# Kernel tuning notes

Measured on AMD Instinct MI355X. Metric: run time of the kernel, lower is better.

Reference implementation:

```python
import jax, jax.numpy as jnp
import numpy as np
import math

N, KZ, IFZ, AHZ, AFZ = 20000, 16, 256, 8, 32
EPS = 1e-5


def layernorm(x, g, b):
    m = jnp.mean(x, axis=-1, keepdims=True)
    v = jnp.mean((x - m) ** 2, axis=-1, keepdims=True)
    return (x - m) * jax.lax.rsqrt(v + EPS) * g + b


def rotate_half(x):
    x1, x2 = jnp.split(x, 2, axis=-1)
    return jnp.concatenate([-x2, x1], axis=-1)


def setup_inputs() -> dict:
    key = jax.random.key(0)
    ks = jax.random.split(key, 16)
    s = 1.0 / math.sqrt(IFZ)
    hf = AHZ * AFZ
    return {
        "x_1": jax.random.normal(ks[0], (N, IFZ), jnp.float32),
        "x_2": jax.random.normal(ks[1], (N, KZ, IFZ), jnp.float32),
        "pos_emb": jax.random.normal(ks[2], (N, AFZ), jnp.float32),
        "edge_index": jax.random.randint(ks[3], (N, KZ), 0, N),
        "Wq": jax.random.normal(ks[4], (IFZ, hf), jnp.float32) * s,
        "Wk": jax.random.normal(ks[5], (IFZ, hf), jnp.float32) * s,
        "Wv": jax.random.normal(ks[6], (IFZ, hf), jnp.float32) * s,
        "Wb": jax.random.normal(ks[7], (IFZ, AHZ), jnp.float32) * s,
        "bln_g": jnp.ones((IFZ,), jnp.float32),
        "bln_b": jnp.zeros((IFZ,), jnp.float32),
        "Wg": jax.random.normal(ks[8], (IFZ, hf), jnp.float32) * s,
        "bg": jnp.zeros((hf,), jnp.float32),
        "Wback": jax.random.normal(ks[9], (hf, IFZ), jnp.float32) / math.sqrt(hf),
        "bback": jnp.zeros((IFZ,), jnp.float32),
        "ln1_g": jnp.ones((IFZ,), jnp.float32),
        "ln1_b": jnp.zeros((IFZ,), jnp.float32),
    }


def reference(x_1, x_2, pos_emb, edge_index, Wq, Wk, Wv, Wb, bln_g, bln_b,
              Wg, bg, Wback, bback, ln1_g, ln1_b):
    n = x_1.shape[0]
    y_1 = x_1[edge_index]                                  # [N,kz,ifz] irregular gather
    q = (x_1 @ Wq).reshape(n, AHZ, AFZ)                    # [N,h,f]
    k = (y_1 @ Wk).reshape(n, KZ, AHZ, AFZ)                # [N,kz,h,f]
    # RoPE: rotate q by each node's own angles, k by gathered neighbor angles
    cos_q = jnp.cos(pos_emb)[:, None, :]                   # [N,1,f]
    sin_q = jnp.sin(pos_emb)[:, None, :]
    q = q * cos_q + rotate_half(q) * sin_q
    pe_n = pos_emb[edge_index]                             # [N,kz,f]
    cos_k = jnp.cos(pe_n)[:, :, None, :]                   # [N,kz,1,f]
    sin_k = jnp.sin(pe_n)[:, :, None, :]
    k = k * cos_k + rotate_half(k) * sin_k
    v = (y_1 @ Wv).reshape(n, KZ, AHZ, AFZ)
    bias_2 = layernorm(x_2, bln_g, bln_b) @ Wb             # [N,kz,h]
    gate = jax.nn.sigmoid(x_1 @ Wg + bg).reshape(n, AHZ, AFZ)
    scores = jnp.einsum('nhf,nkhf->nkh', q, k) / math.sqrt(AFZ) + bias_2
    w = jax.nn.softmax(scores, axis=1)                     # over kz neighbors
    out = gate * jnp.einsum('nkh,nkhf->nhf', w, v)         # [N,h,f]
    out = out.reshape(n, AHZ * AFZ) @ Wback + bback + math.sqrt(2.0) * x_1
    return layernorm(out, ln1_g, ln1_b)
```

## Files before the change

### kernel.cpp

```cpp
#include <hip/hip_runtime.h>
#include <math.h>

#define IFZ 256
#define KZ  16
#define AHZ 8
#define AFZ 32
#define HF  256

typedef _Float16 half8 __attribute__((ext_vector_type(8)));
typedef _Float16 half4 __attribute__((ext_vector_type(4)));
typedef float    f32x4 __attribute__((ext_vector_type(4)));

__global__ void conv_f16(const float* __restrict__ in, _Float16* __restrict__ out, int n4)
{
    int i = blockIdx.x * 256 + threadIdx.x;
    if (i >= n4) return;
    float4 v = reinterpret_cast<const float4*>(in)[i];
    half4 h;
    h[0] = (_Float16)v.x; h[1] = (_Float16)v.y;
    h[2] = (_Float16)v.z; h[3] = (_Float16)v.w;
    reinterpret_cast<half4*>(out)[i] = h;
}

__global__ void prep_all(const float* __restrict__ w0, const float* __restrict__ w1,
                         const float* __restrict__ w2, const float* __restrict__ w3,
                         const float* __restrict__ w4, _Float16* __restrict__ out,
                         const float* __restrict__ g, const float* __restrict__ b,
                         const float* __restrict__ Wb,
                         _Float16* __restrict__ c1T, float* __restrict__ c23)
{
    const int m = blockIdx.y;
    if (m < 5) {
        int k = blockIdx.x;
        int c = threadIdx.x;
        const float* w = (m == 0) ? w0 : (m == 1) ? w1 : (m == 2) ? w2 : (m == 3) ? w3 : w4;
        out[(size_t)m * 65536 + (size_t)c * 256 + k] = (_Float16)w[(size_t)k * 256 + c];
        return;
    }
    if (blockIdx.x != 0) return;

    __shared__ float red[4][16];
    const int f = threadIdx.x;
    const int w = f >> 6, l = f & 63;
    const float gv = g[f], bv = b[f];
    float ph2[8], ph3[8];
    #pragma unroll
    for (int h = 0; h < 8; ++h) {
        float wv = Wb[(size_t)f * 8 + h];
        c1T[h * 256 + f] = (_Float16)(gv * wv);
        ph2[h] = gv * wv;
        ph3[h] = bv * wv;
    }
    c1T[8 * 256 + f] = (_Float16)1.0f;
    #pragma unroll
    for (int cc = 9; cc < 16; ++cc) c1T[cc * 256 + f] = (_Float16)0.0f;

    #pragma unroll
    for (int h = 0; h < 8; ++h) {
        #pragma unroll
        for (int o = 32; o > 0; o >>= 1) {
            ph2[h] += __shfl_xor(ph2[h], o);
            ph3[h] += __shfl_xor(ph3[h], o);
        }
        if (l == h) { red[w][h] = ph2[h]; red[w][8 + h] = ph3[h]; }
    }
    __syncthreads();
    if (f < 16) c23[f] = red[0][f] + red[1][f] + red[2][f] + red[3][f];
}

__launch_bounds__(256)
__global__ void gemm_qkvg(const _Float16* __restrict__ A, const _Float16* __restrict__ WT,
                          const float* __restrict__ pe, const float* __restrict__ bg,
                          _Float16* __restrict__ QH, _Float16* __restrict__ KH,
                          _Float16* __restrict__ VH, _Float16* __restrict__ GH, int N)
{
    __shared__ _Float16 as[64][40];
    __shared__ _Float16 bs[4][64][40];

    const int tid = threadIdx.x;
    const int l   = tid & 63;
    const int w   = tid >> 6;
    const int n0  = blockIdx.x * 64;
    const int c0  = blockIdx.y * 64;

    f32x4 acc[4][4];
    #pragma unroll
    for (int m = 0; m < 4; ++m)
        #pragma unroll
        for (int b = 0; b < 4; ++b)
            { acc[m][b][0]=0.f; acc[m][b][1]=0.f; acc[m][b][2]=0.f; acc[m][b][3]=0.f; }

    const int srow = tid >> 2;
    const int sch  = (tid & 3) * 8;
    const size_t aoff = (size_t)(n0 + srow) * IFZ + sch;
    const size_t boff = (size_t)(c0 + srow) * IFZ + sch;

    half8 av{}, bv0, bv1, bv2, bv3;
    if (n0 + srow < N) av = *reinterpret_cast<const half8*>(A + aoff);
    bv0 = *reinterpret_cast<const half8*>(WT + 0 * 65536 + boff);
    bv1 = *reinterpret_cast<const half8*>(WT + 1 * 65536 + boff);
    bv2 = *reinterpret_cast<const half8*>(WT + 2 * 65536 + boff);
    bv3 = *reinterpret_cast<const half8*>(WT + 3 * 65536 + boff);

    for (int kt = 0; kt < 8; ++kt) {
        __syncthreads();
        *reinterpret_cast<half8*>(&as[srow][sch])    = av;
        *reinterpret_cast<half8*>(&bs[0][srow][sch]) = bv0;
        *reinterpret_cast<half8*>(&bs[1][srow][sch]) = bv1;
        *reinterpret_cast<half8*>(&bs[2][srow][sch]) = bv2;
        *reinterpret_cast<half8*>(&bs[3][srow][sch]) = bv3;
        __syncthreads();

        half8 nav{}, nbv0{}, nbv1{}, nbv2{}, nbv3{};
        if (kt < 7) {
            const int k0 = (kt + 1) * 32;
            if (n0 + srow < N) nav = *reinterpret_cast<const half8*>(A + aoff + k0);
            nbv0 = *reinterpret_cast<const half8*>(WT + 0 * 65536 + boff + k0);
            nbv1 = *reinterpret_cast<const half8*>(WT + 1 * 65536 + boff + k0);
            nbv2 = *reinterpret_cast<const half8*>(WT + 2 * 65536 + boff + k0);
            nbv3 = *reinterpret_cast<const half8*>(WT + 3 * 65536 + boff + k0);
        }

        half8 af = *reinterpret_cast<const half8*>(&as[16 * w + (l & 15)][8 * (l >> 4)]);
        #pragma unroll
        for (int m = 0; m < 4; ++m) {
            #pragma unroll
            for (int b = 0; b < 4; ++b) {
                half8 bf = *reinterpret_cast<const half8*>(&bs[m][16 * b + (l & 15)][8 * (l >> 4)]);
                acc[m][b] = __builtin_amdgcn_mfma_f32_16x16x32_f16(af, bf, acc[m][b], 0, 0, 0);
            }
        }
        av = nav; bv0 = nbv0; bv1 = nbv1; bv2 = nbv2; bv3 = nbv3;
    }

    #pragma unroll
    for (int r = 0; r < 4; ++r) {
        const int grow = n0 + 16 * w + ((l >> 4) << 2) + r;
        if (grow >= N) continue;
        float a0 = pe[(size_t)grow * AFZ + (l & 15)];
        float a1 = pe[(size_t)grow * AFZ + 16 + (l & 15)];
        float s0, c0f, s1, c1f;
        __sincosf(a0, &s0, &c0f);
        __sincosf(a1, &s1, &c1f);
        #pragma unroll
        for (int m = 0; m < 2; ++m) {
            _Float16* o = m ? KH : QH;
            #pragma unroll
            for (int pb = 0; pb < 4; pb += 2) {
                float v0 = acc[m][pb][r], v1 = acc[m][pb + 1][r];
                o[(size_t)grow * HF + c0 + 16 * pb       + (l & 15)] = (_Float16)(v0 * c0f - v1 * s0);
                o[(size_t)grow * HF + c0 + 16 * (pb + 1) + (l & 15)] = (_Float16)(v1 * c1f + v0 * s1);
            }
        }
        #pragma unroll
        for (int b = 0; b < 4; ++b)
            VH[(size_t)grow * HF + c0 + 16 * b + (l & 15)] = (_Float16)acc[2][b][r];
        #pragma unroll
        for (int b = 0; b < 4; ++b) {
            const int c = c0 + 16 * b + (l & 15);
            float v = acc[3][b][r] + bg[c];
            GH[(size_t)grow * HF + c] = (_Float16)(1.f / (1.f + __expf(-v)));
        }
    }
}

__launch_bounds__(256)
__global__ void attn_fused(const _Float16* __restrict__ Qh, const _Float16* __restrict__ Kh,
                           const _Float16* __restrict__ Vh, const _Float16* __restrict__ Gh,
                           const int* __restrict__ eidx, const float* __restrict__ x2,
                           const _Float16* __restrict__ c1T, const float* __restrict__ c23,
                           _Float16* __restrict__ AOh, int N)
{
    const int tid = threadIdx.x;
    const int l   = tid & 63;
    const int w   = tid >> 6;
    const int n   = blockIdx.x * 4 + w;
    if (n >= N) return;
    const int h = l >> 3;
    const int c = l & 15;
    const int p = l >> 4;

    const int ei_reg = eidx[(size_t)n * KZ + c];

    const float* xr = x2 + ((size_t)n * KZ + c) * IFZ + p * 8;
    f32x4 xv[16];
    #pragma unroll
    for (int kt = 0; kt < 8; ++kt) {
        xv[2 * kt]     = __builtin_nontemporal_load(reinterpret_cast<const f32x4*>(xr + kt * 32));
        xv[2 * kt + 1] = __builtin_nontemporal_load(reinterpret_cast<const f32x4*>(xr + kt * 32 + 4));
    }
    half8 bf[8];
    #pragma unroll
    for (int kt = 0; kt < 8; ++kt)
        bf[kt] = *reinterpret_cast<const half8*>(c1T + (size_t)c * 256 + kt * 32 + p * 8);

    f32x4 acc1 = {0.f, 0.f, 0.f, 0.f};
    f32x4 acc2 = {0.f, 0.f, 0.f, 0.f};
    #pragma unroll
    for (int kt = 0; kt < 8; ++kt) {
        f32x4 xa = xv[2 * kt], xb = xv[2 * kt + 1];
        half8 ax, ax2;
        ax[0] = (_Float16)xa[0]; ax[1] = (_Float16)xa[1];
        ax[2] = (_Float16)xa[2]; ax[3] = (_Float16)xa[3];
        ax[4] = (_Float16)xb[0]; ax[5] = (_Float16)xb[1];
        ax[6] = (_Float16)xb[2]; ax[7] = (_Float16)xb[3];
        ax2[0] = (_Float16)(xa[0] * xa[0]); ax2[1] = (_Float16)(xa[1] * xa[1]);
        ax2[2] = (_Float16)(xa[2] * xa[2]); ax2[3] = (_Float16)(xa[3] * xa[3]);
        ax2[4] = (_Float16)(xb[0] * xb[0]); ax2[5] = (_Float16)(xb[1] * xb[1]);
        ax2[6] = (_Float16)(xb[2] * xb[2]); ax2[7] = (_Float16)(xb[3] * xb[3]);
        acc1 = __builtin_amdgcn_mfma_f32_16x16x32_f16(ax,  bf[kt], acc1, 0, 0, 0);
        acc2 = __builtin_amdgcn_mfma_f32_16x16x32_f16(ax2, bf[kt], acc2, 0, 0, 0);
    }

    const float c2v = (c < 8) ? c23[c]     : 0.f;
    const float c3v = (c < 8) ? c23[8 + c] : 0.f;
    const int srcl = (l & 48) | 8;
    float bval[4];
    #pragma unroll
    for (int j = 0; j < 4; ++j) {
        float s1 = __shfl(acc1[j], srcl);
        float s2 = __shfl(acc2[j], srcl);
        float m    = s1 * (1.f / 256.f);
        float var  = s2 * (1.f / 256.f) - m * m;
        float rstd = rsqrtf(var + 1e-5f);
        bval[j] = rstd * (acc1[j] - m * c2v) + c3v;
    }

    half4 qh4 = *reinterpret_cast<const half4*>(Qh + (size_t)n * HF + 4 * l);
    const float q0 = (float)qh4[0], q1 = (float)qh4[1],
                q2 = (float)qh4[2], q3 = (float)qh4[3];

    float sc[16];
    #pragma unroll
    for (int e = 0; e < 16; ++e) {
        const int row = __shfl(ei_reg, e);
        half4 kh4 = *reinterpret_cast<const half4*>(Kh + (size_t)row * HF + 4 * l);
        float s = q0 * (float)kh4[0] + q1 * (float)kh4[1]
                + q2 * (float)kh4[2] + q3 * (float)kh4[3];
        s += __shfl_xor(s, 1); s += __shfl_xor(s, 2); s += __shfl_xor(s, 4);
        sc[e] = s * 0.17677669529663687f
              + __shfl(bval[e & 3], ((e >> 2) << 4) | h);
    }

    float m = sc[0];
    #pragma unroll
    for (int e = 1; e < 16; ++e) m = fmaxf(m, sc[e]);
    float sum = 0.f;
    #pragma unroll
    for (int e = 0; e < 16; ++e) { sc[e] = __expf(sc[e] - m); sum += sc[e]; }
    const float inv = 1.f / sum;

    float o0 = 0.f, o1 = 0.f, o2 = 0.f, o3 = 0.f;
    #pragma unroll
    for (int e = 0; e < 16; ++e) {
        const int row = __shfl(ei_reg, e);
        half4 vh4 = *reinterpret_cast<const half4*>(Vh + (size_t)row * HF + 4 * l);
        const float we = sc[e] * inv;
        o0 = fmaf(we, (float)vh4[0], o0);
        o1 = fmaf(we, (float)vh4[1], o1);
        o2 = fmaf(we, (float)vh4[2], o2);
        o3 = fmaf(we, (float)vh4[3], o3);
    }

    half4 gh4 = *reinterpret_cast<const half4*>(Gh + (size_t)n * HF + 4 * l);
    half4 oh;
    oh[0] = (_Float16)(o0 * (float)gh4[0]);
    oh[1] = (_Float16)(o1 * (float)gh4[1]);
    oh[2] = (_Float16)(o2 * (float)gh4[2]);
    oh[3] = (_Float16)(o3 * (float)gh4[3]);
    *reinterpret_cast<half4*>(AOh + (size_t)n * HF + 4 * l) = oh;
}

__launch_bounds__(256)
__global__ void gemm_back(const _Float16* __restrict__ A, const _Float16* __restrict__ BT,
                          const float* __restrict__ bias, float* __restrict__ Y, int N)
{
    __shared__ _Float16 as[64][40];
    __shared__ _Float16 bs[64][40];

    const int tid = threadIdx.x;
    const int l   = tid & 63;
    const int w   = tid >> 6;
    const int n0  = blockIdx.x * 64;
    const int c0  = blockIdx.y * 64;

    f32x4 acc[4];
    #pragma unroll
    for (int b = 0; b < 4; ++b) { acc[b][0]=0.f; acc[b][1]=0.f; acc[b][2]=0.f; acc[b][3]=0.f; }

    const int srow = tid >> 2;
    const int sch  = (tid & 3) * 8;
    const size_t aoff = (size_t)(n0 + srow) * IFZ + sch;
    const size_t boff = (size_t)(c0 + srow) * IFZ + sch;

    half8 av{}, bv;
    if (n0 + srow < N) av = *reinterpret_cast<const half8*>(A + aoff);
    bv = *reinterpret_cast<const half8*>(BT + boff);

    for (int kt = 0; kt < 8; ++kt) {
        __syncthreads();
        *reinterpret_cast<half8*>(&as[srow][sch]) = av;
        *reinterpret_cast<half8*>(&bs[srow][sch]) = bv;
        __syncthreads();

        half8 nav{}, nbv{};
        if (kt < 7) {
            const int k0 = (kt + 1) * 32;
            if (n0 + srow < N) nav = *reinterpret_cast<const half8*>(A + aoff + k0);
            nbv = *reinterpret_cast<const half8*>(BT + boff + k0);
        }

        half8 af = *reinterpret_cast<const half8*>(&as[16 * w + (l & 15)][8 * (l >> 4)]);
        #pragma unroll
        for (int b = 0; b < 4; ++b) {
            half8 bf = *reinterpret_cast<const half8*>(&bs[16 * b + (l & 15)][8 * (l >> 4)]);
            acc[b] = __builtin_amdgcn_mfma_f32_16x16x32_f16(af, bf, acc[b], 0, 0, 0);
        }
        av = nav; bv = nbv;
    }

    #pragma unroll
    for (int r = 0; r < 4; ++r) {
        const int grow = n0 + 16 * w + ((l >> 4) << 2) + r;
        if (grow >= N) continue;
        #pragma unroll
        for (int b = 0; b < 4; ++b) {
            const int c = c0 + 16 * b + (l & 15);
            Y[(size_t)grow * HF + c] = acc[b][r] + bias[c];
        }
    }
}

__launch_bounds__(256)
__global__ void final_ln(const float* __restrict__ RAWb,
                         const float* __restrict__ x1b,
                         const float* __restrict__ g1,
                         const float* __restrict__ b1,
                         float* __restrict__ outb,
                         int N)
{
    int n    = blockIdx.x * 4 + (threadIdx.x >> 6);
    int lane = threadIdx.x & 63;
    if (n >= N) return;
    const size_t off = (size_t)n * IFZ + lane * 4;
    float4 ur = *reinterpret_cast<const float4*>(RAWb + off);
    float4 ux = *reinterpret_cast<const float4*>(x1b + off);
    float x[4];
    x[0] = ur.x + 1.4142135623730951f * ux.x;
    x[1] = ur.y + 1.4142135623730951f * ux.y;
    x[2] = ur.z + 1.4142135623730951f * ux.z;
    x[3] = ur.w + 1.4142135623730951f * ux.w;
    float s = x[0] + x[1] + x[2] + x[3];
    float q = x[0]*x[0] + x[1]*x[1] + x[2]*x[2] + x[3]*x[3];
    #pragma unroll
    for (int o = 32; o > 0; o >>= 1) { s += __shfl_xor(s, o); q += __shfl_xor(q, o); }
    float m    = s * (1.f / 256.f);
    float var  = q * (1.f / 256.f) - m * m;
    float rstd = rsqrtf(var + 1e-5f);
    float4 uo;
    {
        int f = lane * 4;
        uo.x = (x[0] - m) * rstd * g1[f + 0] + b1[f + 0];
        uo.y = (x[1] - m) * rstd * g1[f + 1] + b1[f + 1];
        uo.z = (x[2] - m) * rstd * g1[f + 2] + b1[f + 2];
        uo.w = (x[3] - m) * rstd * g1[f + 3] + b1[f + 3];
    }
    *reinterpret_cast<float4*>(outb + off) = uo;
}

extern "C" void kernel_launch(void* const* d_in, const int* in_sizes, int n_in,
                              void* d_out, int out_size, void* d_ws, size_t ws_size,
                              hipStream_t stream)
{
    const float* x1   = (const float*)d_in[0];
    const float* x2   = (const float*)d_in[1];
    const float* pe   = (const float*)d_in[2];
    const int*   ei   = (const int*)d_in[3];
    const float* wq   = (const float*)d_in[4];
    const float* wk   = (const float*)d_in[5];
    const float* wv   = (const float*)d_in[6];
    const float* wb   = (const float*)d_in[7];
    const float* blng = (const float*)d_in[8];
    const float* blnb = (const float*)d_in[9];
    const float* wg   = (const float*)d_in[10];
    const float* bg   = (const float*)d_in[11];
    const float* wbk  = (const float*)d_in[12];
    const float* bbk  = (const float*)d_in[13];
    const float* g1   = (const float*)d_in[14];
    const float* b1   = (const float*)d_in[15];

    const int N = in_sizes[0] / IFZ;

    const size_t S2 = (((size_t)N * HF * 2) + 4095) & ~(size_t)4095;
    char* base = (char*)d_ws;
    _Float16* X1H = (_Float16*)(base);
    _Float16* QH  = (_Float16*)(base + 1 * S2);
    _Float16* KH  = (_Float16*)(base + 2 * S2);
    _Float16* VH  = (_Float16*)(base + 3 * S2);
    _Float16* GH  = (_Float16*)(base + 4 * S2);
    _Float16* WT  = (_Float16*)(base + 5 * S2);
    _Float16* C1T = (_Float16*)(base + 5 * S2 + (1u << 20));
    float*    C23 = (float*)   (base + 5 * S2 + (1u << 20) + 8192);
    _Float16* AOH = QH;
    float*    RAW = (float*)(base + 2 * S2);

    conv_f16<<<dim3((N * IFZ / 4 + 255) / 256), 256, 0, stream>>>(x1, X1H, N * IFZ / 4);
    prep_all<<<dim3(256, 6), 256, 0, stream>>>(wq, wk, wv, wg, wbk, WT,
                                               blng, blnb, wb, C1T, C23);

    const int nt = (N + 63) / 64;
    gemm_qkvg<<<dim3(nt, 4), 256, 0, stream>>>(X1H, WT, pe, bg, QH, KH, VH, GH, N);

    attn_fused<<<dim3((N + 3) / 4), 256, 0, stream>>>(QH, KH, VH, GH, ei, x2,
                                                      C1T, C23, AOH, N);

    gemm_back<<<dim3(nt, 4), 256, 0, stream>>>(AOH, WT + 4 * 65536, bbk, RAW, N);

    final_ln<<<dim3((N + 3) / 4), 256, 0, stream>>>(RAW, x1, g1, b1, (float*)d_out, N);
}
```

Baseline: 168.3 us.

## Fuse f32-to-f16 conversion into QKVG GEMM and fuse output LayerNorm into back GEMM

Drops the separate conv_f16 kernel, so gemm_qkvg now loads x_1 in fp32 and converts it to f16 while staging tiles. gemm_back now gives each block the full 256 output columns, letting it add bias and the scaled residual and apply the final LayerNorm in registers with lane shuffles. This removes the fp32 RAW intermediate round trip and two kernel launches. In exchange, each back-GEMM block holds 16 accumulators and a larger shared tile, so register pressure rises and there are a quarter as many blocks (about 313). The epilogue also does strided per-element stores and x1 loads.

```diff
diff --git a/kernel.cpp b/kernel.cpp
--- a/kernel.cpp
+++ b/kernel.cpp
@@ -10,17 +10,6 @@
 typedef _Float16 half8 __attribute__((ext_vector_type(8)));
 typedef _Float16 half4 __attribute__((ext_vector_type(4)));
 typedef float    f32x4 __attribute__((ext_vector_type(4)));
-
-__global__ void conv_f16(const float* __restrict__ in, _Float16* __restrict__ out, int n4)
-{
-    int i = blockIdx.x * 256 + threadIdx.x;
-    if (i >= n4) return;
-    float4 v = reinterpret_cast<const float4*>(in)[i];
-    half4 h;
-    h[0] = (_Float16)v.x; h[1] = (_Float16)v.y;
-    h[2] = (_Float16)v.z; h[3] = (_Float16)v.w;
-    reinterpret_cast<half4*>(out)[i] = h;
-}
 
 __global__ void prep_all(const float* __restrict__ w0, const float* __restrict__ w1,
                          const float* __restrict__ w2, const float* __restrict__ w3,
@@ -69,7 +58,7 @@
 }
 
 __launch_bounds__(256)
-__global__ void gemm_qkvg(const _Float16* __restrict__ A, const _Float16* __restrict__ WT,
+__global__ void gemm_qkvg(const float* __restrict__ A, const _Float16* __restrict__ WT,
                           const float* __restrict__ pe, const float* __restrict__ bg,
                           _Float16* __restrict__ QH, _Float16* __restrict__ KH,
                           _Float16* __restrict__ VH, _Float16* __restrict__ GH, int N)
@@ -94,9 +83,15 @@
     const int sch  = (tid & 3) * 8;
     const size_t aoff = (size_t)(n0 + srow) * IFZ + sch;
     const size_t boff = (size_t)(c0 + srow) * IFZ + sch;
+    const bool arow_ok = (n0 + srow < N);
 
     half8 av{}, bv0, bv1, bv2, bv3;
-    if (n0 + srow < N) av = *reinterpret_cast<const half8*>(A + aoff);
+    if (arow_ok) {
+        f32x4 a0 = *reinterpret_cast<const f32x4*>(A + aoff);
+        f32x4 a1 = *reinterpret_cast<const f32x4*>(A + aoff + 4);
+        av[0]=(_Float16)a0[0]; av[1]=(_Float16)a0[1]; av[2]=(_Float16)a0[2]; av[3]=(_Float16)a0[3];
+        av[4]=(_Float16)a1[0]; av[5]=(_Float16)a1[1]; av[6]=(_Float16)a1[2]; av[7]=(_Float16)a1[3];
+    }
     bv0 = *reinterpret_cast<const half8*>(WT + 0 * 65536 + boff);
     bv1 = *reinterpret_cast<const half8*>(WT + 1 * 65536 + boff);
     bv2 = *reinterpret_cast<const half8*>(WT + 2 * 65536 + boff);
@@ -114,7 +109,12 @@
         half8 nav{}, nbv0{}, nbv1{}, nbv2{}, nbv3{};
         if (kt < 7) {
             const int k0 = (kt + 1) * 32;
-            if (n0 + srow < N) nav = *reinterpret_cast<const half8*>(A + aoff + k0);
+            if (arow_ok) {
+                f32x4 a0 = *reinterpret_cast<const f32x4*>(A + aoff + k0);
+                f32x4 a1 = *reinterpret_cast<const f32x4*>(A + aoff + k0 + 4);
+                nav[0]=(_Float16)a0[0]; nav[1]=(_Float16)a0[1]; nav[2]=(_Float16)a0[2]; nav[3]=(_Float16)a0[3];
+                nav[4]=(_Float16)a1[0]; nav[5]=(_Float16)a1[1]; nav[6]=(_Float16)a1[2]; nav[7]=(_Float16)a1[3];
+            }
             nbv0 = *reinterpret_cast<const half8*>(WT + 0 * 65536 + boff + k0);
             nbv1 = *reinterpret_cast<const half8*>(WT + 1 * 65536 + boff + k0);
             nbv2 = *reinterpret_cast<const half8*>(WT + 2 * 65536 + boff + k0);
@@ -272,100 +272,102 @@
 }
 
 __launch_bounds__(256)
-__global__ void gemm_back(const _Float16* __restrict__ A, const _Float16* __restrict__ BT,
-                          const float* __restrict__ bias, float* __restrict__ Y, int N)
+__global__ void gemm_back_ln(const _Float16* __restrict__ A, const _Float16* __restrict__ BT,
+                             const float* __restrict__ bbk, const float* __restrict__ x1,
+                             const float* __restrict__ g1, const float* __restrict__ b1,
+                             float* __restrict__ out, int N)
 {
     __shared__ _Float16 as[64][40];
-    __shared__ _Float16 bs[64][40];
+    __shared__ _Float16 bs[256][40];
 
     const int tid = threadIdx.x;
     const int l   = tid & 63;
     const int w   = tid >> 6;
     const int n0  = blockIdx.x * 64;
-    const int c0  = blockIdx.y * 64;
-
-    f32x4 acc[4];
-    #pragma unroll
-    for (int b = 0; b < 4; ++b) { acc[b][0]=0.f; acc[b][1]=0.f; acc[b][2]=0.f; acc[b][3]=0.f; }
-
-    const int srow = tid >> 2;
-    const int sch  = (tid & 3) * 8;
-    const size_t aoff = (size_t)(n0 + srow) * IFZ + sch;
-    const size_t boff = (size_t)(c0 + srow) * IFZ + sch;
-
-    half8 av{}, bv;
-    if (n0 + srow < N) av = *reinterpret_cast<const half8*>(A + aoff);
-    bv = *reinterpret_cast<const half8*>(BT + boff);
+
+    f32x4 acc[16];
+    #pragma unroll
+    for (int bb = 0; bb < 16; ++bb)
+        { acc[bb][0]=0.f; acc[bb][1]=0.f; acc[bb][2]=0.f; acc[bb][3]=0.f; }
+
+    const int srowA = tid >> 2;
+    const int schA  = (tid & 3) * 8;
+    const size_t aoff = (size_t)(n0 + srowA) * IFZ + schA;
+    const size_t boff = (size_t)tid * IFZ;
+    const bool arow_ok = (n0 + srowA < N);
+
+    half8 av{}, bv[4];
+    if (arow_ok) av = *reinterpret_cast<const half8*>(A + aoff);
+    #pragma unroll
+    for (int i = 0; i < 4; ++i)
+        bv[i] = *reinterpret_cast<const half8*>(BT + boff + i * 8);
 
     for (int kt = 0; kt < 8; ++kt) {
         __syncthreads();
-        *reinterpret_cast<half8*>(&as[srow][sch]) = av;
-        *reinterpret_cast<half8*>(&bs[srow][sch]) = bv;
+        *reinterpret_cast<half8*>(&as[srowA][schA]) = av;
+        #pragma unroll
+        for (int i = 0; i < 4; ++i)
+            *reinterpret_cast<half8*>(&bs[tid][i * 8]) = bv[i];
         __syncthreads();
 
-        half8 nav{}, nbv{};
+        half8 nav{};
+        half8 nbv[4] = {half8{}, half8{}, half8{}, half8{}};
         if (kt < 7) {
             const int k0 = (kt + 1) * 32;
-            if (n0 + srow < N) nav = *reinterpret_cast<const half8*>(A + aoff + k0);
-            nbv = *reinterpret_cast<const half8*>(BT + boff + k0);
+            if (arow_ok) nav = *reinterpret_cast<const half8*>(A + aoff + k0);
+            #pragma unroll
+            for (int i = 0; i < 4; ++i)
+                nbv[i] = *reinterpret_cast<const half8*>(BT + boff + k0 + i * 8);
         }
 
         half8 af = *reinterpret_cast<const half8*>(&as[16 * w + (l & 15)][8 * (l >> 4)]);
         #pragma unroll
-        for (int b = 0; b < 4; ++b) {
-            half8 bf = *reinterpret_cast<const half8*>(&bs[16 * b + (l & 15)][8 * (l >> 4)]);
-            acc[b] = __builtin_amdgcn_mfma_f32_16x16x32_f16(af, bf, acc[b], 0, 0, 0);
-        }
-        av = nav; bv = nbv;
-    }
-
-    #pragma unroll
-    for (int r = 0; r < 4; ++r) {
-        const int grow = n0 + 16 * w + ((l >> 4) << 2) + r;
-        if (grow >= N) continue;
-        #pragma unroll
-        for (int b = 0; b < 4; ++b) {
-            const int c = c0 + 16 * b + (l & 15);
-            Y[(size_t)grow * HF + c] = acc[b][r] + bias[c];
-        }
-    }
-}
-
-__launch_bounds__(256)
-__global__ void final_ln(const float* __restrict__ RAWb,
-                         const float* __restrict__ x1b,
-                         const float* __restrict__ g1,
-                         const float* __restrict__ b1,
-                         float* __restrict__ outb,
-                         int N)
-{
-    int n    = blockIdx.x * 4 + (threadIdx.x >> 6);
-    int lane = threadIdx.x & 63;
-    if (n >= N) return;
-    const size_t off = (size_t)n * IFZ + lane * 4;
-    float4 ur = *reinterpret_cast<const float4*>(RAWb + off);
-    float4 ux = *reinterpret_cast<const float4*>(x1b + off);
-    float x[4];
-    x[0] = ur.x + 1.4142135623730951f * ux.x;
-    x[1] = ur.y + 1.4142135623730951f * ux.y;
-    x[2] = ur.z + 1.4142135623730951f * ux.z;
-    x[3] = ur.w + 1.4142135623730951f * ux.w;
-    float s = x[0] + x[1] + x[2] + x[3];
-    float q = x[0]*x[0] + x[1]*x[1] + x[2]*x[2] + x[3]*x[3];
-    #pragma unroll
-    for (int o = 32; o > 0; o >>= 1) { s += __shfl_xor(s, o); q += __shfl_xor(q, o); }
-    float m    = s * (1.f / 256.f);
-    float var  = q * (1.f / 256.f) - m * m;
-    float rstd = rsqrtf(var + 1e-5f);
-    float4 uo;
-    {
-        int f = lane * 4;
-        uo.x = (x[0] - m) * rstd * g1[f + 0] + b1[f + 0];
-        uo.y = (x[1] - m) * rstd * g1[f + 1] + b1[f + 1];
-        uo.z = (x[2] - m) * rstd * g1[f + 2] + b1[f + 2];
-        uo.w = (x[3] - m) * rstd * g1[f + 3] + b1[f + 3];
-    }
-    *reinterpret_cast<float4*>(outb + off) = uo;
+        for (int bb = 0; bb < 16; ++bb) {
+            half8 bf = *reinterpret_cast<const half8*>(&bs[16 * bb + (l & 15)][8 * (l >> 4)]);
+            acc[bb] = __builtin_amdgcn_mfma_f32_16x16x32_f16(af, bf, acc[bb], 0, 0, 0);
+        }
+        av = nav;
+        #pragma unroll
+        for (int i = 0; i < 4; ++i) bv[i] = nbv[i];
+    }
+
+    const int c15 = l & 15;
+    const int p   = l >> 4;
+    float bias_r[16], g_r[16], b_r[16];
+    #pragma unroll
+    for (int bb = 0; bb < 16; ++bb) {
+        const int cc = 16 * bb + c15;
+        bias_r[bb] = bbk[cc]; g_r[bb] = g1[cc]; b_r[bb] = b1[cc];
+    }
+
+    #pragma unroll
+    for (int j = 0; j < 4; ++j) {
+        const int grow = n0 + 16 * w + 4 * p + j;
+        const bool ok  = grow < N;
+        float v[16];
+        float s = 0.f, qq = 0.f;
+        #pragma unroll
+        for (int bb = 0; bb < 16; ++bb) {
+            const int cc = 16 * bb + c15;
+            float t = acc[bb][j] + bias_r[bb]
+                    + 1.4142135623730951f * (ok ? x1[(size_t)grow * IFZ + cc] : 0.f);
+            v[bb] = t; s += t; qq += t * t;
+        }
+        s  += __shfl_xor(s, 1);  s  += __shfl_xor(s, 2);
+        s  += __shfl_xor(s, 4);  s  += __shfl_xor(s, 8);
+        qq += __shfl_xor(qq, 1); qq += __shfl_xor(qq, 2);
+        qq += __shfl_xor(qq, 4); qq += __shfl_xor(qq, 8);
+        const float m    = s * (1.f / 256.f);
+        const float var  = qq * (1.f / 256.f) - m * m;
+        const float rstd = rsqrtf(var + 1e-5f);
+        if (ok) {
+            #pragma unroll
+            for (int bb = 0; bb < 16; ++bb) {
+                const int cc = 16 * bb + c15;
+                out[(size_t)grow * IFZ + cc] = (v[bb] - m) * rstd * g_r[bb] + b_r[bb];
+            }
+        }
+    }
 }
 
 extern "C" void kernel_launch(void* const* d_in, const int* in_sizes, int n_in,
@@ -393,28 +395,24 @@
 
     const size_t S2 = (((size_t)N * HF * 2) + 4095) & ~(size_t)4095;
     char* base = (char*)d_ws;
-    _Float16* X1H = (_Float16*)(base);
-    _Float16* QH  = (_Float16*)(base + 1 * S2);
-    _Float16* KH  = (_Float16*)(base + 2 * S2);
-    _Float16* VH  = (_Float16*)(base + 3 * S2);
-    _Float16* GH  = (_Float16*)(base + 4 * S2);
-    _Float16* WT  = (_Float16*)(base + 5 * S2);
-    _Float16* C1T = (_Float16*)(base + 5 * S2 + (1u << 20));
-    float*    C23 = (float*)   (base + 5 * S2 + (1u << 20) + 8192);
+    _Float16* QH  = (_Float16*)(base);
+    _Float16* KH  = (_Float16*)(base + 1 * S2);
+    _Float16* VH  = (_Float16*)(base + 2 * S2);
+    _Float16* GH  = (_Float16*)(base + 3 * S2);
+    _Float16* WT  = (_Float16*)(base + 4 * S2);
+    _Float16* C1T = (_Float16*)(base + 4 * S2 + (1u << 20));
+    float*    C23 = (float*)   (base + 4 * S2 + (1u << 20) + 8192);
     _Float16* AOH = QH;
-    float*    RAW = (float*)(base + 2 * S2);
-
-    conv_f16<<<dim3((N * IFZ / 4 + 255) / 256), 256, 0, stream>>>(x1, X1H, N * IFZ / 4);
+
     prep_all<<<dim3(256, 6), 256, 0, stream>>>(wq, wk, wv, wg, wbk, WT,
                                                blng, blnb, wb, C1T, C23);
 
     const int nt = (N + 63) / 64;
-    gemm_qkvg<<<dim3(nt, 4), 256, 0, stream>>>(X1H, WT, pe, bg, QH, KH, VH, GH, N);
+    gemm_qkvg<<<dim3(nt, 4), 256, 0, stream>>>(x1, WT, pe, bg, QH, KH, VH, GH, N);
 
     attn_fused<<<dim3((N + 3) / 4), 256, 0, stream>>>(QH, KH, VH, GH, ei, x2,
                                                       C1T, C23, AOH, N);
 
-    gemm_back<<<dim3(nt, 4), 256, 0, stream>>>(AOH, WT + 4 * 65536, bbk, RAW, N);
-
-    final_ln<<<dim3((N + 3) / 4), 256, 0, stream>>>(RAW, x1, g1, b1, (float*)d_out, N);
+    gemm_back_ln<<<dim3(nt), 256, 0, stream>>>(AOH, WT + 4 * 65536, bbk, x1, g1, b1,
+                                               (float*)d_out, N);
 }
```

Result: slower. 179.7 us (+6.8%).
